# Optimization experiments

Hardware: AMD Instinct MI355X
Metric: run time of the kernel (lower is better)

## Reference

```python
import jax, jax.numpy as jnp
import numpy as np

D_MODEL = 1024
NHEAD = 16
DFF = 4096
MAXD = 32


def _ln(x, g, b, eps=1e-5):
    mu = jnp.mean(x, axis=-1, keepdims=True)
    var = jnp.mean(jnp.square(x - mu), axis=-1, keepdims=True)
    return (x - mu) * jax.lax.rsqrt(var + eps) * g + b


def setup_inputs() -> dict:
    key = jax.random.key(0)
    ks = jax.random.split(key, 16)
    D, F, H = D_MODEL, DFF, NHEAD
    s = 1.0 / np.sqrt(D)
    inp = {
        "src": jax.random.normal(ks[0], (2, 2048, D), dtype=jnp.float32),
        "Wq": jax.random.normal(ks[1], (D, D), dtype=jnp.float32) * s,
        "Wk": jax.random.normal(ks[2], (D, D), dtype=jnp.float32) * s,
        "Wv": jax.random.normal(ks[3], (D, D), dtype=jnp.float32) * s,
        "bq": jnp.zeros((D,), jnp.float32),
        "bk": jnp.zeros((D,), jnp.float32),
        "bv": jnp.zeros((D,), jnp.float32),
        "Wo": jax.random.normal(ks[4], (D, D), dtype=jnp.float32) * s,
        "bo": jnp.zeros((D,), jnp.float32),
        "rpe_table": jax.random.normal(ks[5], (2 * MAXD + 1, H), dtype=jnp.float32) * 0.02,
        "W1": jax.random.normal(ks[6], (D, F), dtype=jnp.float32) * s,
        "b1": jnp.zeros((F,), jnp.float32),
        "W2": jax.random.normal(ks[7], (F, D), dtype=jnp.float32) * (1.0 / np.sqrt(F)),
        "b2": jnp.zeros((D,), jnp.float32),
        "ln1_g": jnp.ones((D,), jnp.float32),
        "ln1_b": jnp.zeros((D,), jnp.float32),
        "ln2_g": jnp.ones((D,), jnp.float32),
        "ln2_b": jnp.zeros((D,), jnp.float32),
    }
    return inp


def reference(src, Wq, Wk, Wv, bq, bk, bv, Wo, bo, rpe_table, W1, b1, W2, b2,
              ln1_g, ln1_b, ln2_g, ln2_b):
    B, L, D = src.shape
    H = NHEAD
    Dh = D // H
    scale = 1.0 / jnp.sqrt(jnp.asarray(Dh, src.dtype))

    # relative position bias: [L, L, H] -> [H, L, L]
    pos = jnp.arange(L)
    rel = jnp.clip(pos[None, :] - pos[:, None], -MAXD, MAXD) + MAXD  # [L, L]
    bias = jnp.transpose(rpe_table[rel], (2, 0, 1))  # [H, L, L]

    q = (src @ Wq + bq).reshape(B, L, H, Dh)
    k = (src @ Wk + bk).reshape(B, L, H, Dh)
    v = (src @ Wv + bv).reshape(B, L, H, Dh)

    scores = jnp.einsum("blhd,bmhd->bhlm", q, k) * scale + bias[None]
    attn = jax.nn.softmax(scores, axis=-1)
    ctx = jnp.einsum("bhlm,bmhd->blhd", attn, v).reshape(B, L, D)
    attn_out = ctx @ Wo + bo

    x = _ln(src + attn_out, ln1_g, ln1_b)
    ff = jax.nn.relu(x @ W1 + b1) @ W2 + b2
    return _ln(x + ff, ln2_g, ln2_b)
```

## Files before the change

kernel.cpp:

```cpp
#include <hip/hip_runtime.h>
#include <hip/hip_bf16.h>

#define D_MODEL 1024
#define NHEAD 16
#define DH 64
#define DFF 4096
#define MAXD 32
#define L_ 2048
#define NROW 4096

typedef __attribute__((ext_vector_type(4))) float floatx4;
typedef __attribute__((ext_vector_type(8))) __bf16 bf16x8;
typedef __attribute__((ext_vector_type(4))) unsigned short ushort4v;

static __device__ inline unsigned short f2bf(float f) {
    __hip_bfloat16 h = __float2bfloat16(f);
    return __builtin_bit_cast(unsigned short, h);
}

static __device__ inline floatx4 mfma16(bf16x8 a, bf16x8 b, floatx4 c) {
    return __builtin_amdgcn_mfma_f32_16x16x32_bf16(a, b, c, 0, 0, 0);
}

static __device__ inline void gload_lds16(const unsigned short* g, unsigned short* l) {
    __builtin_amdgcn_global_load_lds((const __attribute__((address_space(1))) unsigned int*)g,
                                     (__attribute__((address_space(3))) unsigned int*)l,
                                     16, 0, 0);
}

__global__ __launch_bounds__(256) void cast_bf16_kernel(const float* __restrict__ in,
                                                        unsigned short* __restrict__ out, int n4) {
    int i = blockIdx.x * 256 + threadIdx.x;
    if (i < n4) {
        floatx4 v = *(const floatx4*)&in[(size_t)i * 4];
        ushort4v o;
        o.x = f2bf(v[0]); o.y = f2bf(v[1]); o.z = f2bf(v[2]); o.w = f2bf(v[3]);
        *(ushort4v*)&out[(size_t)i * 4] = o;
    }
}

__global__ __launch_bounds__(256) void transpose_cast_kernel(const float* __restrict__ W,
                                                             unsigned short* __restrict__ WT,
                                                             int K, int N) {
    __shared__ float tile[32][33];
    int k0 = blockIdx.y * 32, n0 = blockIdx.x * 32;
    for (int i = threadIdx.x; i < 1024; i += 256) {
        int r = i >> 5, c = i & 31;
        tile[r][c] = W[(size_t)(k0 + r) * N + n0 + c];
    }
    __syncthreads();
    for (int i = threadIdx.x; i < 1024; i += 256) {
        int r = i >> 5, c = i & 31;
        WT[(size_t)(n0 + r) * K + k0 + c] = f2bf(tile[c][r]);
    }
}

__global__ __launch_bounds__(256) void pack_bias_kernel(const float* __restrict__ bq,
                                                        const float* __restrict__ bk,
                                                        const float* __restrict__ bv,
                                                        float* __restrict__ out) {
    int i = blockIdx.x * 256 + threadIdx.x;
    if (i < 3072) out[i] = (i < 1024) ? bq[i] : ((i < 2048) ? bk[i - 1024] : bv[i - 2048]);
}

template <int NF, bool OUTBF16, bool RELU>
__global__ __launch_bounds__(256) void gemm_kernel(const unsigned short* __restrict__ A,
                                                   const unsigned short* __restrict__ BT,
                                                   const float* __restrict__ bias,
                                                   void* __restrict__ Cout,
                                                   int M, int N, int K, int gx) {
    constexpr int BN = NF * 32;
    __shared__ unsigned short Asm[128][64];
    __shared__ unsigned short Bsm[BN][64];
    int t = threadIdx.x;
    int lane = t & 63, w = t >> 6;
    int wm = w >> 1, wn = w & 1;
    int lr = lane & 15, hg = lane >> 4;

    int nwg = gridDim.x;
    int bid = blockIdx.x;
    int id = (bid & 7) * (nwg >> 3) + (bid >> 3);
    int m0 = (id / gx) * 128, n0 = (id % gx) * BN;

    floatx4 acc[4][NF];
#pragma unroll
    for (int i = 0; i < 4; i++)
#pragma unroll
        for (int j = 0; j < NF; j++) acc[i][j] = (floatx4)0.0f;

    const int lr7 = lr & 7;

    for (int k0 = 0; k0 < K; k0 += 64) {
        __syncthreads();
#pragma unroll
        for (int i = 0; i < 4; i++) {
            int c = t + i * 256;
            int r = c >> 3, ch = c & 7;
            int chs = ch ^ (r & 7);
            gload_lds16(&A[(size_t)(m0 + r) * K + k0 + chs * 8], &Asm[r][ch * 8]);
        }
#pragma unroll
        for (int i = 0; i < BN / 32; i++) {
            int c = t + i * 256;
            int r = c >> 3, ch = c & 7;
            int chs = ch ^ (r & 7);
            gload_lds16(&BT[(size_t)(n0 + r) * K + k0 + chs * 8], &Bsm[r][ch * 8]);
        }
        __syncthreads();
#pragma unroll
        for (int kc = 0; kc < 2; kc++) {
            int ch = (kc * 4 + hg) ^ lr7;
            bf16x8 af[4], bfg[NF];
#pragma unroll
            for (int mf = 0; mf < 4; mf++)
                af[mf] = *(const bf16x8*)&Asm[wm * 64 + mf * 16 + lr][ch * 8];
#pragma unroll
            for (int nf = 0; nf < NF; nf++)
                bfg[nf] = *(const bf16x8*)&Bsm[wn * NF * 16 + nf * 16 + lr][ch * 8];
#pragma unroll
            for (int mf = 0; mf < 4; mf++)
#pragma unroll
                for (int nf = 0; nf < NF; nf++) acc[mf][nf] = mfma16(af[mf], bfg[nf], acc[mf][nf]);
        }
    }

#pragma unroll
    for (int mf = 0; mf < 4; mf++)
#pragma unroll
        for (int nf = 0; nf < NF; nf++) {
            int col = n0 + wn * NF * 16 + nf * 16 + lr;
            float bv = bias[col];
#pragma unroll
            for (int r = 0; r < 4; r++) {
                int row = m0 + wm * 64 + mf * 16 + hg * 4 + r;
                float v = acc[mf][nf][r] + bv;
                if (RELU) v = v > 0.f ? v : 0.f;
                if (OUTBF16)
                    ((unsigned short*)Cout)[(size_t)row * N + col] = f2bf(v);
                else
                    ((float*)Cout)[(size_t)row * N + col] = v;
            }
        }
}

__global__ __launch_bounds__(512, 4) void attn_kernel(const unsigned short* __restrict__ qkv,
                                                      const float* __restrict__ rpe,
                                                      unsigned short* __restrict__ ctx) {
    __shared__ unsigned short Kb0[64 * 64];
    __shared__ unsigned short Kb1[64 * 64];
    __shared__ unsigned short Vt[64 * 64];
    __shared__ unsigned short Ps[8][16 * 64];
    __shared__ float rpl[65];

    const int t = threadIdx.x;
    const int lane = t & 63, w = t >> 6;
    const int lr = lane & 15, hg = lane >> 4;
    const int lrs = (lr & 7) ^ (lr >> 3);

    const int g = blockIdx.x;
    const int blk = (g & 7) * 64 + (g >> 3);
    const int qb = blk & 15;
    const int h = (blk >> 4) & 15;
    const int b = blk >> 8;
    const int q0 = qb * 128;
    const int hcol = h * 64;
    const size_t rowbase = (size_t)b * L_ * 3072;

    const int kr = t >> 3, kch = t & 7;
    const int kswz = (kch ^ (kr & 7) ^ (kr >> 3)) & 7;
    unsigned short* kdst0 = &Kb0[kr * 64 + kch * 8];
    unsigned short* kdst1 = &Kb1[kr * 64 + kch * 8];

    if (t < 65) rpl[t] = rpe[t * NHEAD + h];

    const int qi = q0 + w * 16 + lr;
    bf16x8 qf0 = *(const bf16x8*)&qkv[rowbase + (size_t)qi * 3072 + hcol + hg * 8];
    bf16x8 qf1 = *(const bf16x8*)&qkv[rowbase + (size_t)qi * 3072 + hcol + 32 + hg * 8];

    gload_lds16(&qkv[rowbase + (size_t)kr * 3072 + 1024 + hcol + kswz * 8], kdst0);
    __syncthreads();

    float rpl0 = rpl[0], rpl64 = rpl[64];
    floatx4 o[4];
#pragma unroll
    for (int df = 0; df < 4; df++) o[df] = (floatx4)0.f;
    float mst = -1e30f, lst = 0.f;
    const float scale = 0.125f;
    unsigned short* PsW = &Ps[w][0];

#define ATT_STEP(KT, KcP, KnP, MORE)                                                               \
    {                                                                                              \
        const int key0 = (KT) * 64;                                                                \
        int4 tv = *(const int4*)&qkv[rowbase + (size_t)(key0 + kr) * 3072 + 2048 + hcol + kch * 8];\
        if (MORE)                                                                                  \
            gload_lds16(&qkv[rowbase + (size_t)(key0 + 64 + kr) * 3072 + 1024 + hcol + kswz * 8],  \
                        KnP);                                                                      \
        floatx4 st[4];                                                                             \
        _Pragma("unroll")                                                                          \
        for (int kf = 0; kf < 4; kf++) {                                                           \
            int sw = lrs ^ (kf * 2);                                                               \
            bf16x8 a0 = *(const bf16x8*)&(KcP)[(kf * 16 + lr) * 64 + ((hg ^ sw) << 3)];            \
            bf16x8 a1 = *(const bf16x8*)&(KcP)[(kf * 16 + lr) * 64 + (((4 + hg) ^ sw) << 3)];      \
            st[kf] = mfma16(a1, qf1, mfma16(a0, qf0, (floatx4)0.f));                               \
        }                                                                                          \
        bool rightC = (key0 > q0 + 159);                                                           \
        bool leftC = (key0 + 95 < q0);                                                             \
        float cbv = rightC ? rpl64 : rpl0;                                                         \
        float sv[16];                                                                              \
        float mx = -1e30f;                                                                         \
        if (leftC || rightC) {                                                                     \
            _Pragma("unroll")                                                                      \
            for (int kf = 0; kf < 4; kf++)                                                         \
                _Pragma("unroll")                                                                  \
                for (int r = 0; r < 4; r++) {                                                      \
                    float v = st[kf][r] * scale + cbv;                                             \
                    sv[kf * 4 + r] = v;                                                            \
                    mx = fmaxf(mx, v);                                                             \
                }                                                                                  \
        } else {                                                                                   \
            _Pragma("unroll")                                                                      \
            for (int kf = 0; kf < 4; kf++)                                                         \
                _Pragma("unroll")                                                                  \
                for (int r = 0; r < 4; r++) {                                                      \
                    int rel = key0 + kf * 16 + hg * 4 + r - qi;                                    \
                    rel = rel < -MAXD ? -MAXD : (rel > MAXD ? MAXD : rel);                         \
                    float v = st[kf][r] * scale + rpl[rel + MAXD];                                 \
                    sv[kf * 4 + r] = v;                                                            \
                    mx = fmaxf(mx, v);                                                             \
                }                                                                                  \
        }                                                                                          \
        mx = fmaxf(mx, __shfl_xor(mx, 16, 64));                                                    \
        mx = fmaxf(mx, __shfl_xor(mx, 32, 64));                                                    \
        float newm = fmaxf(mst, mx);                                                               \
        float corr = __expf(mst - newm);                                                           \
        mst = newm;                                                                                \
        float ps = 0.f;                                                                            \
        unsigned int pk[8];                                                                        \
        _Pragma("unroll")                                                                          \
        for (int kf = 0; kf < 4; kf++)                                                             \
            _Pragma("unroll")                                                                      \
            for (int j = 0; j < 2; j++) {                                                          \
                float p0 = __expf(sv[kf * 4 + 2 * j] - newm);                                      \
                float p1 = __expf(sv[kf * 4 + 2 * j + 1] - newm);                                  \
                ps += p0 + p1;                                                                     \
                pk[kf * 2 + j] = (unsigned int)f2bf(p0) | ((unsigned int)f2bf(p1) << 16);          \
            }                                                                                      \
        lst = lst * corr + ps;                                                                     \
        _Pragma("unroll")                                                                          \
        for (int df = 0; df < 4; df++) o[df] *= corr;                                              \
        _Pragma("unroll")                                                                          \
        for (int kf = 0; kf < 4; kf++)                                                             \
            _Pragma("unroll")                                                                      \
            for (int j = 0; j < 2; j++) {                                                          \
                int ch = ((kf * 2 + (hg >> 1)) ^ lrs) & 7;                                         \
                *(unsigned int*)&PsW[lr * 64 + (ch << 3) + (hg & 1) * 4 + 2 * j] = pk[kf * 2 + j]; \
            }                                                                                      \
        _Pragma("unroll")                                                                          \
        for (int e = 0; e < 8; e++) {                                                              \
            int d = kch * 8 + e;                                                                   \
            int ch = ((kr >> 3) ^ e ^ kch) & 7;                                                    \
            unsigned short val = (unsigned short)(((const unsigned int*)&tv)[e >> 1] >>            \
                                                  ((e & 1) * 16));                                 \
            Vt[d * 64 + (ch << 3) + (kr & 7)] = val;                                               \
        }                                                                                          \
        __syncthreads();                                                                           \
        bf16x8 pb0 = *(const bf16x8*)&PsW[lr * 64 + ((hg ^ lrs) << 3)];                            \
        bf16x8 pb1 = *(const bf16x8*)&PsW[lr * 64 + (((4 + hg) ^ lrs) << 3)];                      \
        _Pragma("unroll")                                                                          \
        for (int df = 0; df < 4; df++) {                                                           \
            int sw = lrs ^ (df * 2);                                                               \
            bf16x8 v0 = *(const bf16x8*)&Vt[(df * 16 + lr) * 64 + ((hg ^ sw) << 3)];               \
            bf16x8 v1 = *(const bf16x8*)&Vt[(df * 16 + lr) * 64 + (((4 + hg) ^ sw) << 3)];         \
            o[df] = mfma16(v1, pb1, mfma16(v0, pb0, o[df]));                                       \
        }                                                                                          \
        __syncthreads();                                                                           \
    }

    for (int kt = 0; kt < L_ / 64; kt += 2) {
        ATT_STEP(kt, Kb0, kdst1, true);
        ATT_STEP(kt + 1, Kb1, kdst0, (kt + 2 < L_ / 64));
    }
#undef ATT_STEP

    float rs = lst;
    rs += __shfl_xor(rs, 16, 64);
    rs += __shfl_xor(rs, 32, 64);
    float inv = 1.f / rs;
    size_t obase = (size_t)(b * L_ + qi) * 1024 + hcol;
#pragma unroll
    for (int df = 0; df < 4; df++)
#pragma unroll
        for (int r = 0; r < 4; r++)
            ctx[obase + df * 16 + hg * 4 + r] = f2bf(o[df][r] * inv);
}

template <bool WBF>
__global__ __launch_bounds__(256) void resln_kernel(const float* __restrict__ ra,
                                                    const float* __restrict__ rb,
                                                    const float* __restrict__ g,
                                                    const float* __restrict__ be,
                                                    float* __restrict__ outf,
                                                    unsigned short* __restrict__ outb) {
    __shared__ float red[4];
    __shared__ float red2[4];
    int row = blockIdx.x;
    int t = threadIdx.x;
    int w = t >> 6, lane = t & 63;
    size_t base = (size_t)row * 1024 + t * 4;
    floatx4 a = *(const floatx4*)&ra[base];
    floatx4 b = *(const floatx4*)&rb[base];
    floatx4 y = a + b;
    float s = y[0] + y[1] + y[2] + y[3];
#pragma unroll
    for (int d = 1; d < 64; d <<= 1) s += __shfl_xor(s, d, 64);
    if (lane == 0) red[w] = s;
    __syncthreads();
    float mu = (red[0] + red[1] + red[2] + red[3]) * (1.f / 1024.f);
    floatx4 d4 = y - mu;
    float sq = d4[0] * d4[0] + d4[1] * d4[1] + d4[2] * d4[2] + d4[3] * d4[3];
#pragma unroll
    for (int d = 1; d < 64; d <<= 1) sq += __shfl_xor(sq, d, 64);
    if (lane == 0) red2[w] = sq;
    __syncthreads();
    float var = (red2[0] + red2[1] + red2[2] + red2[3]) * (1.f / 1024.f);
    float rstd = rsqrtf(var + 1e-5f);
    floatx4 gg = *(const floatx4*)&g[t * 4];
    floatx4 bb = *(const floatx4*)&be[t * 4];
    floatx4 outv;
#pragma unroll
    for (int i = 0; i < 4; i++) outv[i] = d4[i] * rstd * gg[i] + bb[i];
    *(floatx4*)&outf[base] = outv;
    if (WBF) {
        ushort4v ov;
        ov.x = f2bf(outv[0]); ov.y = f2bf(outv[1]); ov.z = f2bf(outv[2]); ov.w = f2bf(outv[3]);
        *(ushort4v*)&outb[base] = ov;
    }
}

extern "C" void kernel_launch(void* const* d_in, const int* in_sizes, int n_in,
                              void* d_out, int out_size, void* d_ws, size_t ws_size,
                              hipStream_t stream) {
    const float* src = (const float*)d_in[0];
    const float* Wq = (const float*)d_in[1];
    const float* Wk = (const float*)d_in[2];
    const float* Wv = (const float*)d_in[3];
    const float* bq = (const float*)d_in[4];
    const float* bk = (const float*)d_in[5];
    const float* bv = (const float*)d_in[6];
    const float* Wo = (const float*)d_in[7];
    const float* bo = (const float*)d_in[8];
    const float* rpe = (const float*)d_in[9];
    const float* W1 = (const float*)d_in[10];
    const float* b1 = (const float*)d_in[11];
    const float* W2 = (const float*)d_in[12];
    const float* b2 = (const float*)d_in[13];
    const float* ln1g = (const float*)d_in[14];
    const float* ln1b = (const float*)d_in[15];
    const float* ln2g = (const float*)d_in[16];
    const float* ln2b = (const float*)d_in[17];
    float* out = (float*)d_out;
    char* ws = (char*)d_ws;

    const size_t o_srcb = 0;
    const size_t o_wtqkv = o_srcb + 8388608;
    const size_t o_wto = o_wtqkv + 6291456;
    const size_t o_wt1 = o_wto + 2097152;
    const size_t o_wt2 = o_wt1 + 8388608;
    const size_t o_bqkv = o_wt2 + 8388608;
    const size_t o_qkv = o_bqkv + 12288;
    const size_t o_ctxb = o_qkv + 25165824;
    const size_t o_x = o_ctxb + 8388608;
    const size_t o_hb = o_x + 16777216;

    unsigned short* srcb = (unsigned short*)(ws + o_srcb);
    unsigned short* wtqkv = (unsigned short*)(ws + o_wtqkv);
    unsigned short* wto = (unsigned short*)(ws + o_wto);
    unsigned short* wt1 = (unsigned short*)(ws + o_wt1);
    unsigned short* wt2 = (unsigned short*)(ws + o_wt2);
    float* bqkv = (float*)(ws + o_bqkv);
    unsigned short* qkvb = (unsigned short*)(ws + o_qkv);
    unsigned short* ctxb = (unsigned short*)(ws + o_ctxb);
    float* x = (float*)(ws + o_x);
    unsigned short* hb = (unsigned short*)(ws + o_hb);
    float* attnout = (float*)(ws + o_qkv);
    float* ff = (float*)(ws + o_qkv);
    unsigned short* xb = (unsigned short*)(ws + o_srcb);

    cast_bf16_kernel<<<4096, 256, 0, stream>>>(src, srcb, 1048576);
    transpose_cast_kernel<<<dim3(32, 32), 256, 0, stream>>>(Wq, wtqkv, 1024, 1024);
    transpose_cast_kernel<<<dim3(32, 32), 256, 0, stream>>>(Wk, wtqkv + 1024 * 1024, 1024, 1024);
    transpose_cast_kernel<<<dim3(32, 32), 256, 0, stream>>>(Wv, wtqkv + 2 * 1024 * 1024, 1024, 1024);
    transpose_cast_kernel<<<dim3(32, 32), 256, 0, stream>>>(Wo, wto, 1024, 1024);
    transpose_cast_kernel<<<dim3(128, 32), 256, 0, stream>>>(W1, wt1, 1024, 4096);
    transpose_cast_kernel<<<dim3(32, 128), 256, 0, stream>>>(W2, wt2, 4096, 1024);
    pack_bias_kernel<<<12, 256, 0, stream>>>(bq, bk, bv, bqkv);

    gemm_kernel<4, true, false><<<768, 256, 0, stream>>>(srcb, wtqkv, bqkv, qkvb, NROW, 3072, 1024, 24);
    attn_kernel<<<512, 512, 0, stream>>>(qkvb, rpe, ctxb);
    gemm_kernel<2, false, false><<<512, 256, 0, stream>>>(ctxb, wto, bo, attnout, NROW, 1024, 1024, 16);
    resln_kernel<true><<<4096, 256, 0, stream>>>(src, attnout, ln1g, ln1b, x, xb);
    gemm_kernel<4, true, true><<<1024, 256, 0, stream>>>(xb, wt1, b1, hb, NROW, 4096, 1024, 32);
    gemm_kernel<2, false, false><<<512, 256, 0, stream>>>(hb, wt2, b2, ff, NROW, 1024, 4096, 16);
    resln_kernel<false><<<4096, 256, 0, stream>>>(x, ff, ln2g, ln2b, out, nullptr);
}
```

Measured before the change: 305.9 us.

## Process two 16-row query tiles per wave in attention to reuse K/V tiles

Each attention wave now handles 32 query rows (two 16-row groups) instead of 16, so every block covers 256 queries and the grid halves to 256 blocks. Each K and V tile staged in shared memory is reused across twice as many queries, which halves global K/V traffic and the transpose work per query. The cost is more registers per wave (two output accumulators and two softmax states), a serialized P staging through the same per-wave buffer, and only 256 blocks, which may underfill the GPU's compute units.

```diff
diff --git a/kernel.cpp b/kernel.cpp
--- a/kernel.cpp
+++ b/kernel.cpp
@@ -158,11 +158,11 @@
     const int lrs = (lr & 7) ^ (lr >> 3);
 
     const int g = blockIdx.x;
-    const int blk = (g & 7) * 64 + (g >> 3);
-    const int qb = blk & 15;
-    const int h = (blk >> 4) & 15;
-    const int b = blk >> 8;
-    const int q0 = qb * 128;
+    const int blk = (g & 7) * 32 + (g >> 3);
+    const int qb = blk & 7;
+    const int h = (blk >> 3) & 15;
+    const int b = blk >> 7;
+    const int q0 = qb * 256;
     const int hcol = h * 64;
     const size_t rowbase = (size_t)b * L_ * 3072;
 
@@ -173,18 +173,21 @@
 
     if (t < 65) rpl[t] = rpe[t * NHEAD + h];
 
-    const int qi = q0 + w * 16 + lr;
-    bf16x8 qf0 = *(const bf16x8*)&qkv[rowbase + (size_t)qi * 3072 + hcol + hg * 8];
-    bf16x8 qf1 = *(const bf16x8*)&qkv[rowbase + (size_t)qi * 3072 + hcol + 32 + hg * 8];
+    const int qiA = q0 + w * 32 + lr;
+    const int qiB = qiA + 16;
+    bf16x8 qfA0 = *(const bf16x8*)&qkv[rowbase + (size_t)qiA * 3072 + hcol + hg * 8];
+    bf16x8 qfA1 = *(const bf16x8*)&qkv[rowbase + (size_t)qiA * 3072 + hcol + 32 + hg * 8];
+    bf16x8 qfB0 = *(const bf16x8*)&qkv[rowbase + (size_t)qiB * 3072 + hcol + hg * 8];
+    bf16x8 qfB1 = *(const bf16x8*)&qkv[rowbase + (size_t)qiB * 3072 + hcol + 32 + hg * 8];
 
     gload_lds16(&qkv[rowbase + (size_t)kr * 3072 + 1024 + hcol + kswz * 8], kdst0);
     __syncthreads();
 
     float rpl0 = rpl[0], rpl64 = rpl[64];
-    floatx4 o[4];
-#pragma unroll
-    for (int df = 0; df < 4; df++) o[df] = (floatx4)0.f;
-    float mst = -1e30f, lst = 0.f;
+    floatx4 oA[4], oB[4];
+#pragma unroll
+    for (int df = 0; df < 4; df++) { oA[df] = (floatx4)0.f; oB[df] = (floatx4)0.f; }
+    float mstA = -1e30f, lstA = 0.f, mstB = -1e30f, lstB = 0.f;
     const float scale = 0.125f;
     unsigned short* PsW = &Ps[w][0];
 
@@ -195,66 +198,111 @@
         if (MORE)                                                                                  \
             gload_lds16(&qkv[rowbase + (size_t)(key0 + 64 + kr) * 3072 + 1024 + hcol + kswz * 8],  \
                         KnP);                                                                      \
-        floatx4 st[4];                                                                             \
+        floatx4 stA[4], stB[4];                                                                    \
         _Pragma("unroll")                                                                          \
         for (int kf = 0; kf < 4; kf++) {                                                           \
             int sw = lrs ^ (kf * 2);                                                               \
             bf16x8 a0 = *(const bf16x8*)&(KcP)[(kf * 16 + lr) * 64 + ((hg ^ sw) << 3)];            \
             bf16x8 a1 = *(const bf16x8*)&(KcP)[(kf * 16 + lr) * 64 + (((4 + hg) ^ sw) << 3)];      \
-            st[kf] = mfma16(a1, qf1, mfma16(a0, qf0, (floatx4)0.f));                               \
-        }                                                                                          \
-        bool rightC = (key0 > q0 + 159);                                                           \
+            stA[kf] = mfma16(a1, qfA1, mfma16(a0, qfA0, (floatx4)0.f));                            \
+            stB[kf] = mfma16(a1, qfB1, mfma16(a0, qfB0, (floatx4)0.f));                            \
+        }                                                                                          \
+        bool rightC = (key0 > q0 + 287);                                                           \
         bool leftC = (key0 + 95 < q0);                                                             \
+        bool ccp = leftC || rightC;                                                                \
         float cbv = rightC ? rpl64 : rpl0;                                                         \
-        float sv[16];                                                                              \
-        float mx = -1e30f;                                                                         \
-        if (leftC || rightC) {                                                                     \
+        unsigned int pk1[8];                                                                       \
+                                                                     \
+        {                                                                                          \
+            float sv[16];                                                                          \
+            float mx = -1e30f;                                                                     \
+            if (ccp) {                                                                             \
+                _Pragma("unroll")                                                                  \
+                for (int kf = 0; kf < 4; kf++)                                                     \
+                    _Pragma("unroll")                                                              \
+                    for (int r = 0; r < 4; r++) {                                                  \
+                        float v = stA[kf][r] * scale + cbv;                                        \
+                        sv[kf * 4 + r] = v;                                                        \
+                        mx = fmaxf(mx, v);                                                         \
+                    }                                                                              \
+            } else {                                                                               \
+                _Pragma("unroll")                                                                  \
+                for (int kf = 0; kf < 4; kf++)                                                     \
+                    _Pragma("unroll")                                                              \
+                    for (int r = 0; r < 4; r++) {                                                  \
+                        int rel = key0 + kf * 16 + hg * 4 + r - qiA;                               \
+                        rel = rel < -MAXD ? -MAXD : (rel > MAXD ? MAXD : rel);                     \
+                        float v = stA[kf][r] * scale + rpl[rel + MAXD];                            \
+                        sv[kf * 4 + r] = v;                                                        \
+                        mx = fmaxf(mx, v);                                                         \
+                    }                                                                              \
+            }                                                                                      \
+            mx = fmaxf(mx, __shfl_xor(mx, 16, 64));                                                \
+            mx = fmaxf(mx, __shfl_xor(mx, 32, 64));                                                \
+            float newm = fmaxf(mstA, mx);                                                          \
+            float corr = __expf(mstA - newm);                                                      \
+            mstA = newm;                                                                           \
+            float ps = 0.f;                                                                        \
             _Pragma("unroll")                                                                      \
             for (int kf = 0; kf < 4; kf++)                                                         \
                 _Pragma("unroll")                                                                  \
-                for (int r = 0; r < 4; r++) {                                                      \
-                    float v = st[kf][r] * scale + cbv;                                             \
-                    sv[kf * 4 + r] = v;                                                            \
-                    mx = fmaxf(mx, v);                                                             \
+                for (int j = 0; j < 2; j++) {                                                      \
+                    float p0 = __expf(sv[kf * 4 + 2 * j] - newm);                                  \
+                    float p1 = __expf(sv[kf * 4 + 2 * j + 1] - newm);                              \
+                    ps += p0 + p1;                                                                 \
+                    unsigned int pk = (unsigned int)f2bf(p0) | ((unsigned int)f2bf(p1) << 16);     \
+                    int ch = ((kf * 2 + (hg >> 1)) ^ lrs) & 7;                                     \
+                    *(unsigned int*)&PsW[lr * 64 + (ch << 3) + (hg & 1) * 4 + 2 * j] = pk;         \
                 }                                                                                  \
-        } else {                                                                                   \
+            lstA = lstA * corr + ps;                                                               \
+            _Pragma("unroll")                                                                      \
+            for (int df = 0; df < 4; df++) oA[df] *= corr;                                         \
+        }                                                                                          \
+                                             \
+        {                                                                                          \
+            float sv[16];                                                                          \
+            float mx = -1e30f;                                                                     \
+            if (ccp) {                                                                             \
+                _Pragma("unroll")                                                                  \
+                for (int kf = 0; kf < 4; kf++)                                                     \
+                    _Pragma("unroll")                                                              \
+                    for (int r = 0; r < 4; r++) {                                                  \
+                        float v = stB[kf][r] * scale + cbv;                                        \
+                        sv[kf * 4 + r] = v;                                                        \
+                        mx = fmaxf(mx, v);                                                         \
+                    }                                                                              \
+            } else {                                                                               \
+                _Pragma("unroll")                                                                  \
+                for (int kf = 0; kf < 4; kf++)                                                     \
+                    _Pragma("unroll")                                                              \
+                    for (int r = 0; r < 4; r++) {                                                  \
+                        int rel = key0 + kf * 16 + hg * 4 + r - qiB;                               \
+                        rel = rel < -MAXD ? -MAXD : (rel > MAXD ? MAXD : rel);                     \
+                        float v = stB[kf][r] * scale + rpl[rel + MAXD];                            \
+                        sv[kf * 4 + r] = v;                                                        \
+                        mx = fmaxf(mx, v);                                                         \
+                    }                                                                              \
+            }                                                                                      \
+            mx = fmaxf(mx, __shfl_xor(mx, 16, 64));                                                \
+            mx = fmaxf(mx, __shfl_xor(mx, 32, 64));                                                \
+            float newm = fmaxf(mstB, mx);                                                          \
+            float corr = __expf(mstB - newm);                                                      \
+            mstB = newm;                                                                           \
+            float ps = 0.f;                                                                        \
             _Pragma("unroll")                                                                      \
             for (int kf = 0; kf < 4; kf++)                                                         \
                 _Pragma("unroll")                                                                  \
-                for (int r = 0; r < 4; r++) {                                                      \
-                    int rel = key0 + kf * 16 + hg * 4 + r - qi;                                    \
-                    rel = rel < -MAXD ? -MAXD : (rel > MAXD ? MAXD : rel);                         \
-                    float v = st[kf][r] * scale + rpl[rel + MAXD];                                 \
-                    sv[kf * 4 + r] = v;                                                            \
-                    mx = fmaxf(mx, v);                                                             \
+                for (int j = 0; j < 2; j++) {                                                      \
+                    float p0 = __expf(sv[kf * 4 + 2 * j] - newm);                                  \
+                    float p1 = __expf(sv[kf * 4 + 2 * j + 1] - newm);                              \
+                    ps += p0 + p1;                                                                 \
+                    pk1[kf * 2 + j] = (unsigned int)f2bf(p0) | ((unsigned int)f2bf(p1) << 16);     \
                 }                                                                                  \
-        }                                                                                          \
-        mx = fmaxf(mx, __shfl_xor(mx, 16, 64));                                                    \
-        mx = fmaxf(mx, __shfl_xor(mx, 32, 64));                                                    \
-        float newm = fmaxf(mst, mx);                                                               \
-        float corr = __expf(mst - newm);                                                           \
-        mst = newm;                                                                                \
-        float ps = 0.f;                                                                            \
-        unsigned int pk[8];                                                                        \
-        _Pragma("unroll")                                                                          \
-        for (int kf = 0; kf < 4; kf++)                                                             \
-            _Pragma("unroll")                                                                      \
-            for (int j = 0; j < 2; j++) {                                                          \
-                float p0 = __expf(sv[kf * 4 + 2 * j] - newm);                                      \
-                float p1 = __expf(sv[kf * 4 + 2 * j + 1] - newm);                                  \
-                ps += p0 + p1;                                                                     \
-                pk[kf * 2 + j] = (unsigned int)f2bf(p0) | ((unsigned int)f2bf(p1) << 16);          \
-            }                                                                                      \
-        lst = lst * corr + ps;                                                                     \
-        _Pragma("unroll")                                                                          \
-        for (int df = 0; df < 4; df++) o[df] *= corr;                                              \
-        _Pragma("unroll")                                                                          \
-        for (int kf = 0; kf < 4; kf++)                                                             \
-            _Pragma("unroll")                                                                      \
-            for (int j = 0; j < 2; j++) {                                                          \
-                int ch = ((kf * 2 + (hg >> 1)) ^ lrs) & 7;                                         \
-                *(unsigned int*)&PsW[lr * 64 + (ch << 3) + (hg & 1) * 4 + 2 * j] = pk[kf * 2 + j]; \
-            }                                                                                      \
+            lstB = lstB * corr + ps;                                                               \
+            _Pragma("unroll")                                                                      \
+            for (int df = 0; df < 4; df++) oB[df] *= corr;                                         \
+        }                                                                                          \
+                                                \
         _Pragma("unroll")                                                                          \
         for (int e = 0; e < 8; e++) {                                                              \
             int d = kch * 8 + e;                                                                   \
@@ -264,14 +312,37 @@
             Vt[d * 64 + (ch << 3) + (kr & 7)] = val;                                               \
         }                                                                                          \
         __syncthreads();                                                                           \
-        bf16x8 pb0 = *(const bf16x8*)&PsW[lr * 64 + ((hg ^ lrs) << 3)];                            \
-        bf16x8 pb1 = *(const bf16x8*)&PsW[lr * 64 + (((4 + hg) ^ lrs) << 3)];                      \
+                                                                                \
+        {                                                                                          \
+            bf16x8 pb0 = *(const bf16x8*)&PsW[lr * 64 + ((hg ^ lrs) << 3)];                        \
+            bf16x8 pb1 = *(const bf16x8*)&PsW[lr * 64 + (((4 + hg) ^ lrs) << 3)];                  \
+            _Pragma("unroll")                                                                      \
+            for (int df = 0; df < 4; df++) {                                                       \
+                int sw = lrs ^ (df * 2);                                                           \
+                bf16x8 v0 = *(const bf16x8*)&Vt[(df * 16 + lr) * 64 + ((hg ^ sw) << 3)];           \
+                bf16x8 v1 = *(const bf16x8*)&Vt[(df * 16 + lr) * 64 + (((4 + hg) ^ sw) << 3)];     \
+                oA[df] = mfma16(v1, pb1, mfma16(v0, pb0, oA[df]));                                 \
+            }                                                                                      \
+        }                                                                                          \
+                   \
         _Pragma("unroll")                                                                          \
-        for (int df = 0; df < 4; df++) {                                                           \
-            int sw = lrs ^ (df * 2);                                                               \
-            bf16x8 v0 = *(const bf16x8*)&Vt[(df * 16 + lr) * 64 + ((hg ^ sw) << 3)];               \
-            bf16x8 v1 = *(const bf16x8*)&Vt[(df * 16 + lr) * 64 + (((4 + hg) ^ sw) << 3)];         \
-            o[df] = mfma16(v1, pb1, mfma16(v0, pb0, o[df]));                                       \
+        for (int kf = 0; kf < 4; kf++)                                                             \
+            _Pragma("unroll")                                                                      \
+            for (int j = 0; j < 2; j++) {                                                          \
+                int ch = ((kf * 2 + (hg >> 1)) ^ lrs) & 7;                                         \
+                *(unsigned int*)&PsW[lr * 64 + (ch << 3) + (hg & 1) * 4 + 2 * j] = pk1[kf * 2 + j];\
+            }                                                                                      \
+                                                                                \
+        {                                                                                          \
+            bf16x8 pb0 = *(const bf16x8*)&PsW[lr * 64 + ((hg ^ lrs) << 3)];                        \
+            bf16x8 pb1 = *(const bf16x8*)&PsW[lr * 64 + (((4 + hg) ^ lrs) << 3)];                  \
+            _Pragma("unroll")                                                                      \
+            for (int df = 0; df < 4; df++) {                                                       \
+                int sw = lrs ^ (df * 2);                                                           \
+                bf16x8 v0 = *(const bf16x8*)&Vt[(df * 16 + lr) * 64 + ((hg ^ sw) << 3)];           \
+                bf16x8 v1 = *(const bf16x8*)&Vt[(df * 16 + lr) * 64 + (((4 + hg) ^ sw) << 3)];     \
+                oB[df] = mfma16(v1, pb1, mfma16(v0, pb0, oB[df]));                                 \
+            }                                                                                      \
         }                                                                                          \
         __syncthreads();                                                                           \
     }
@@ -282,16 +353,30 @@
     }
 #undef ATT_STEP
 
-    float rs = lst;
-    rs += __shfl_xor(rs, 16, 64);
-    rs += __shfl_xor(rs, 32, 64);
-    float inv = 1.f / rs;
-    size_t obase = (size_t)(b * L_ + qi) * 1024 + hcol;
-#pragma unroll
-    for (int df = 0; df < 4; df++)
-#pragma unroll
-        for (int r = 0; r < 4; r++)
-            ctx[obase + df * 16 + hg * 4 + r] = f2bf(o[df][r] * inv);
+    {
+        float rs = lstA;
+        rs += __shfl_xor(rs, 16, 64);
+        rs += __shfl_xor(rs, 32, 64);
+        float inv = 1.f / rs;
+        size_t obase = (size_t)(b * L_ + qiA) * 1024 + hcol;
+#pragma unroll
+        for (int df = 0; df < 4; df++)
+#pragma unroll
+            for (int r = 0; r < 4; r++)
+                ctx[obase + df * 16 + hg * 4 + r] = f2bf(oA[df][r] * inv);
+    }
+    {
+        float rs = lstB;
+        rs += __shfl_xor(rs, 16, 64);
+        rs += __shfl_xor(rs, 32, 64);
+        float inv = 1.f / rs;
+        size_t obase = (size_t)(b * L_ + qiB) * 1024 + hcol;
+#pragma unroll
+        for (int df = 0; df < 4; df++)
+#pragma unroll
+            for (int r = 0; r < 4; r++)
+                ctx[obase + df * 16 + hg * 4 + r] = f2bf(oB[df][r] * inv);
+    }
 }
 
 template <bool WBF>
@@ -396,7 +481,7 @@
     pack_bias_kernel<<<12, 256, 0, stream>>>(bq, bk, bv, bqkv);
 
     gemm_kernel<4, true, false><<<768, 256, 0, stream>>>(srcb, wtqkv, bqkv, qkvb, NROW, 3072, 1024, 24);
-    attn_kernel<<<512, 512, 0, stream>>>(qkvb, rpe, ctxb);
+    attn_kernel<<<256, 512, 0, stream>>>(qkvb, rpe, ctxb);
     gemm_kernel<2, false, false><<<512, 256, 0, stream>>>(ctxb, wto, bo, attnout, NROW, 1024, 1024, 16);
     resln_kernel<true><<<4096, 256, 0, stream>>>(src, attnout, ln1g, ln1b, x, xb);
     gemm_kernel<4, true, true><<<1024, 256, 0, stream>>>(xb, wt1, b1, hb, NROW, 4096, 1024, 32);
```

New measurement: 524.7 us. 71.5% more time.
